# Performance work log

Measured on AMD Instinct MI355X. Metric: run time of the kernel, lower is better.

The kernel has to match this reference:

```python
import jax, jax.numpy as jnp
import numpy as np

N_ITER = 50  # bisection iterations (matches entmax_bisect default)


def entmax_bisect(x, alpha):
    """alpha-entmax via bisection along axis=1. x: [B, L, 1], alpha: [1] (>1)."""
    a_m1 = alpha - 1.0
    inv = 1.0 / a_m1
    xs = x * a_m1
    d = x.shape[1]
    max_val = jnp.max(xs, axis=1, keepdims=True)
    tau_lo = max_val - 1.0
    tau_hi = max_val - (1.0 / d) ** a_m1
    f_lo = jnp.sum(jnp.maximum(xs - tau_lo, 0.0) ** inv, axis=1, keepdims=True) - 1.0

    def body(i, carry):
        tau_lo, dm = carry
        dm = dm * 0.5
        tau_m = tau_lo + dm
        f_m = jnp.sum(jnp.maximum(xs - tau_m, 0.0) ** inv, axis=1, keepdims=True) - 1.0
        tau_lo = jnp.where(f_m * f_lo >= 0.0, tau_m, tau_lo)
        return (tau_lo, dm)

    tau_lo, dm = jax.lax.fori_loop(0, N_ITER, body, (tau_lo, tau_hi - tau_lo))
    p = jnp.maximum(xs - (tau_lo + 0.5 * dm), 0.0) ** inv
    return p / jnp.sum(p, axis=1, keepdims=True)


def setup_inputs() -> dict:
    key = jax.random.key(0)
    ks = jax.random.split(key, 8)
    B, L, E2, D = 256, 512, 512, 256  # E2 = emb_size * 2
    C_target = jax.random.normal(ks[0], (B, E2), jnp.float32)
    C = jax.random.normal(ks[1], (B, L, E2), jnp.float32)
    X = jax.random.normal(ks[2], (B, E2, D), jnp.float32)
    alpha = jnp.array([1.5], jnp.float32)  # entmax-1.5
    mask = jax.random.randint(ks[3], (B, L), 0, 2, jnp.int32).at[:, 0].set(1)
    s = 1.0 / np.sqrt(E2)
    Wg1 = jax.random.uniform(ks[4], (E2, E2), jnp.float32, -s, s)
    Wg2 = jax.random.uniform(ks[5], (E2, E2), jnp.float32, -s, s)
    Wg0 = jax.random.uniform(ks[6], (E2, 1), jnp.float32, -s, s)
    bias_alpha = jax.random.normal(ks[7], (E2,), jnp.float32) * 0.02
    return dict(C_target=C_target, C=C, X=X, alpha=alpha, mask=mask,
                Wg1=Wg1, Wg2=Wg2, Wg0=Wg0, bias_alpha=bias_alpha)


def reference(C_target, C, X, alpha, mask, Wg1, Wg2, Wg0, bias_alpha):
    q = C_target[:, None, :]                               # [B, 1, 2E]
    h = jax.nn.relu(C @ Wg1 + q @ Wg2 + bias_alpha)        # [B, L, 2E]
    score = h @ Wg0                                        # [B, L, 1]
    score = jnp.where(mask[..., None] == 0, -1e30, score)  # mask -> -inf
    p = entmax_bisect(score, alpha)                        # sparse attn over L
    attn = jnp.swapaxes(p, 1, 2) @ C                       # [B, 1, 2E]
    out = jnp.sum(attn @ X, axis=1)                        # [B, D]
    return out
```

## Files before the change

kernel.cpp:

```cpp
#include <hip/hip_runtime.h>
#include <hip/hip_bf16.h>

typedef __bf16 bf16_t;
typedef bf16_t bf16x8 __attribute__((ext_vector_type(8)));
typedef float f32x4 __attribute__((ext_vector_type(4)));

__global__ void k_wg1t(const float* __restrict__ Wg1, bf16_t* __restrict__ Wg1T) {
    __shared__ float tile[32][33];
    const int k0 = blockIdx.x * 32;
    const int e0 = blockIdx.y * 32;
    const int tx = threadIdx.x;
    const int ty = threadIdx.y;
    #pragma unroll
    for (int i = 0; i < 32; i += 8)
        tile[ty + i][tx] = Wg1[(k0 + ty + i) * 512 + e0 + tx];
    __syncthreads();
    #pragma unroll
    for (int i = 0; i < 32; i += 8)
        Wg1T[(e0 + ty + i) * 512 + k0 + tx] = (bf16_t)tile[tx][ty + i];
}

__global__ __launch_bounds__(256) void k_gate(const float* __restrict__ Ct,
                                              const float* __restrict__ Wg2,
                                              const float* __restrict__ bias,
                                              float* __restrict__ g) {
    __shared__ float q[512];
    const int b = blockIdx.x;
    const int t = threadIdx.x;
    q[t]       = Ct[b * 512 + t];
    q[t + 256] = Ct[b * 512 + t + 256];
    __syncthreads();
    const int e = (blockIdx.y << 8) + t;
    float acc = bias[e];
    #pragma unroll 8
    for (int k = 0; k < 512; ++k)
        acc = fmaf(q[k], Wg2[k * 512 + e], acc);
    g[b * 512 + e] = acc;
}

__global__ __launch_bounds__(256, 2) void k_score(const float* __restrict__ C,
                                                  const bf16_t* __restrict__ Wg1T,
                                                  const float* __restrict__ g,
                                                  const float* __restrict__ Wg0,
                                                  const int* __restrict__ mask,
                                                  float* __restrict__ score) {
    __shared__ bf16_t As[64 * 32];
    __shared__ bf16_t Bs[512 * 32];
    __shared__ float  sred[4][64];

    const int t    = threadIdx.x;
    const int lane = t & 63;
    const int wave = t >> 6;
    const int quad = lane >> 4;
    const int l15  = lane & 15;
    const int row0 = blockIdx.x * 64;
    const int b    = row0 >> 9;

    f32x4 acc[4][8] = {};

    for (int kc = 0; kc < 512; kc += 32) {
        __syncthreads();
        #pragma unroll
        for (int i = 0; i < 8; ++i) {
            const int f  = i * 256 + t;
            const int r  = f >> 2;
            const int c8 = (f & 3) << 3;
            __builtin_amdgcn_global_load_lds(
                (const __attribute__((address_space(1))) void*)(Wg1T + r * 512 + kc + c8),
                (__attribute__((address_space(3))) void*)(Bs + f * 8), 16, 0, 0);
        }
        #pragma unroll
        for (int i = 0; i < 2; ++i) {
            const int f  = i * 256 + t;
            const int r  = f >> 3;
            const int c4 = (f & 7) << 2;
            const float4 v = *reinterpret_cast<const float4*>(
                &C[(size_t)(row0 + r) * 512 + kc + c4]);
            union { bf16_t h[4]; uint2 u; } pk;
            pk.h[0] = (bf16_t)v.x; pk.h[1] = (bf16_t)v.y;
            pk.h[2] = (bf16_t)v.z; pk.h[3] = (bf16_t)v.w;
            *reinterpret_cast<uint2*>(&As[r * 32 + c4]) = pk.u;
        }
        __syncthreads();
        bf16x8 afr[4], bfr[8];
        #pragma unroll
        for (int mi = 0; mi < 4; ++mi)
            afr[mi] = *reinterpret_cast<const bf16x8*>(
                &As[(mi * 16 + l15) * 32 + quad * 8]);
        #pragma unroll
        for (int ni = 0; ni < 8; ++ni)
            bfr[ni] = *reinterpret_cast<const bf16x8*>(
                &Bs[(wave * 128 + ni * 16 + l15) * 32 + quad * 8]);
        #pragma unroll
        for (int mi = 0; mi < 4; ++mi)
            #pragma unroll
            for (int ni = 0; ni < 8; ++ni)
                acc[mi][ni] = __builtin_amdgcn_mfma_f32_16x16x32_bf16(
                    afr[mi], bfr[ni], acc[mi][ni], 0, 0, 0);
    }

    float rsum[16];
    #pragma unroll
    for (int i = 0; i < 16; ++i) rsum[i] = 0.f;
    #pragma unroll
    for (int ni = 0; ni < 8; ++ni) {
        const int n  = wave * 128 + ni * 16 + l15;
        const float gv = g[(b << 9) + n];
        const float w0 = Wg0[n];
        #pragma unroll
        for (int mi = 0; mi < 4; ++mi)
            #pragma unroll
            for (int r = 0; r < 4; ++r) {
                float u = fmaxf(acc[mi][ni][r] + gv, 0.f);
                rsum[mi * 4 + r] = fmaf(u, w0, rsum[mi * 4 + r]);
            }
    }
    #pragma unroll
    for (int i = 0; i < 16; ++i) {
        float v = rsum[i];
        v += __shfl_xor(v, 1);
        v += __shfl_xor(v, 2);
        v += __shfl_xor(v, 4);
        v += __shfl_xor(v, 8);
        rsum[i] = v;
    }
    if (l15 == 0) {
        #pragma unroll
        for (int mi = 0; mi < 4; ++mi)
            #pragma unroll
            for (int r = 0; r < 4; ++r)
                sred[wave][mi * 16 + quad * 4 + r] = rsum[mi * 4 + r];
    }
    __syncthreads();
    if (t < 64) {
        const float sc = sred[0][t] + sred[1][t] + sred[2][t] + sred[3][t];
        const int grow = row0 + t;
        score[grow] = (mask[grow] == 0) ? -1e30f : sc;
    }
}

__global__ __launch_bounds__(256) void k_entmax(const float* __restrict__ score,
                                                const float* __restrict__ alpha,
                                                float* __restrict__ p) {
    const int wave = threadIdx.x >> 6;
    const int lane = threadIdx.x & 63;
    const int b    = (blockIdx.x << 2) + wave;
    const float am1 = alpha[0] - 1.0f;
    const float inv = 1.0f / am1;
    const bool  sq  = fabsf(inv - 2.0f) < 1e-6f;

    const float* sb = score + (b << 9);
    float x[8];
    {
        const float4 v0 = *reinterpret_cast<const float4*>(sb + lane * 8);
        const float4 v1 = *reinterpret_cast<const float4*>(sb + lane * 8 + 4);
        x[0] = v0.x * am1; x[1] = v0.y * am1; x[2] = v0.z * am1; x[3] = v0.w * am1;
        x[4] = v1.x * am1; x[5] = v1.y * am1; x[6] = v1.z * am1; x[7] = v1.w * am1;
    }
    float m = x[0];
    #pragma unroll
    for (int j = 1; j < 8; ++j) m = fmaxf(m, x[j]);
    #pragma unroll
    for (int s = 1; s < 64; s <<= 1) m = fmaxf(m, __shfl_xor(m, s));

    float tau_lo = m - 1.0f;
    float dm = (m - powf(1.0f / 512.0f, am1)) - tau_lo;

    float f_lo;
    {
        float s = 0.f;
        #pragma unroll
        for (int j = 0; j < 8; ++j) {
            const float u = fmaxf(x[j] - tau_lo, 0.f);
            s += sq ? u * u : powf(u, inv);
        }
        #pragma unroll
        for (int sh = 1; sh < 64; sh <<= 1) s += __shfl_xor(s, sh);
        f_lo = s - 1.0f;
    }
    for (int it = 0; it < 50; ++it) {
        dm *= 0.5f;
        const float tau_m = tau_lo + dm;
        float s = 0.f;
        #pragma unroll
        for (int j = 0; j < 8; ++j) {
            const float u = fmaxf(x[j] - tau_m, 0.f);
            s += sq ? u * u : powf(u, inv);
        }
        #pragma unroll
        for (int sh = 1; sh < 64; sh <<= 1) s += __shfl_xor(s, sh);
        if ((s - 1.0f) * f_lo >= 0.f) tau_lo = tau_m;
    }
    const float tau = tau_lo + 0.5f * dm;
    float pj[8];
    float Z = 0.f;
    #pragma unroll
    for (int j = 0; j < 8; ++j) {
        const float u = fmaxf(x[j] - tau, 0.f);
        pj[j] = sq ? u * u : powf(u, inv);
        Z += pj[j];
    }
    #pragma unroll
    for (int sh = 1; sh < 64; sh <<= 1) Z += __shfl_xor(Z, sh);
    const float rz = 1.0f / Z;
    float4 o0, o1;
    o0.x = pj[0] * rz; o0.y = pj[1] * rz; o0.z = pj[2] * rz; o0.w = pj[3] * rz;
    o1.x = pj[4] * rz; o1.y = pj[5] * rz; o1.z = pj[6] * rz; o1.w = pj[7] * rz;
    *reinterpret_cast<float4*>(p + (b << 9) + lane * 8)     = o0;
    *reinterpret_cast<float4*>(p + (b << 9) + lane * 8 + 4) = o1;
}

__global__ __launch_bounds__(256) void k_attn(const float* __restrict__ p,
                                              const float* __restrict__ C,
                                              float* __restrict__ part) {
    __shared__ float pv_s[128];
    const int b  = blockIdx.x;
    const int ch = blockIdx.y;
    const int t  = threadIdx.x;
    const float* Cb = C + (size_t)b * 512 * 512 + (size_t)ch * 128 * 512;
    const float* pb = p + (b << 9) + (ch << 7);
    if (t < 128) pv_s[t] = pb[t];
    __syncthreads();
    float a0 = 0.f, a1 = 0.f;
    for (int l = 0; l < 128; ++l) {
        const float pv = pv_s[l];
        if (pv != 0.f) {
            a0 = fmaf(pv, Cb[(size_t)l * 512 + t], a0);
            a1 = fmaf(pv, Cb[(size_t)l * 512 + t + 256], a1);
        }
    }
    float* pp = part + (size_t)((b << 2) + ch) * 512;
    pp[t]       = a0;
    pp[t + 256] = a1;
}

__global__ __launch_bounds__(256) void k_out(const float* __restrict__ part,
                                             const float* __restrict__ X,
                                             float* __restrict__ out) {
    __shared__ float as_[128];
    const int b  = blockIdx.x;
    const int ec = blockIdx.y;
    const int t  = threadIdx.x;
    if (t < 128) {
        const int e = (ec << 7) + t;
        const float* pp = part + (size_t)(b << 2) * 512;
        as_[t] = pp[e] + pp[512 + e] + pp[1024 + e] + pp[1536 + e];
    }
    __syncthreads();
    const float* Xb = X + (size_t)b * 512 * 256 + (size_t)(ec << 7) * 256;
    float acc = 0.f;
    #pragma unroll 4
    for (int e = 0; e < 128; ++e)
        acc = fmaf(as_[e], Xb[e * 256 + t], acc);
    atomicAdd(&out[(b << 8) + t], acc);
}

extern "C" void kernel_launch(void* const* d_in, const int* in_sizes, int n_in,
                              void* d_out, int out_size, void* d_ws, size_t ws_size,
                              hipStream_t stream) {
    const float* C_target = (const float*)d_in[0];
    const float* C        = (const float*)d_in[1];
    const float* X        = (const float*)d_in[2];
    const float* alpha    = (const float*)d_in[3];
    const int*   mask     = (const int*)  d_in[4];
    const float* Wg1      = (const float*)d_in[5];
    const float* Wg2      = (const float*)d_in[6];
    const float* Wg0      = (const float*)d_in[7];
    const float* bias     = (const float*)d_in[8];
    float* out = (float*)d_out;

    char* ws = (char*)d_ws;
    bf16_t* wg1t  = (bf16_t*)(ws);
    float*  g     = (float*)(ws + (512u << 10));
    float*  score = (float*)(ws + (1024u << 10));
    float*  p     = (float*)(ws + (1536u << 10));
    float*  part  = (float*)(ws + (2048u << 10));

    k_wg1t  <<<dim3(16, 16), dim3(32, 8), 0, stream>>>(Wg1, wg1t);
    k_gate  <<<dim3(256, 2), 256, 0, stream>>>(C_target, Wg2, bias, g);
    k_score <<<2048, 256, 0, stream>>>(C, wg1t, g, Wg0, mask, score);
    k_entmax<<<64, 256, 0, stream>>>(score, alpha, p);
    k_attn  <<<dim3(256, 4), 256, 0, stream>>>(p, C, part);
    hipMemsetAsync(d_out, 0, (size_t)out_size * sizeof(float), stream);
    k_out   <<<dim3(256, 4), 256, 0, stream>>>(part, X, out);
}
```

Baseline: 593.8 us.

## Skip masked rows in score GEMM and use sparse entmax output for attention

Compacts the unmasked row indices per batch and computes the score GEMM only over those rows, gathering C rows by index. The N dimension is split across two blocks that combine through atomicAdd into a zeroed score buffer. Entmax now applies the mask itself and emits a compacted list of nonzero probabilities, so the attention pass gathers only rows with nonzero weight. This removes about half of the GEMM work, since the mask is random, and most of the C reads in attention. The costs are extra kernels, a memset, atomics and gathered, less regular memory access.

```diff
diff --git a/kernel.cpp b/kernel.cpp
--- a/kernel.cpp
+++ b/kernel.cpp
@@ -38,63 +38,106 @@
     g[b * 512 + e] = acc;
 }
 
-__global__ __launch_bounds__(256, 2) void k_score(const float* __restrict__ C,
+__global__ __launch_bounds__(64) void k_compact(const int* __restrict__ mask,
+                                                int* __restrict__ idx,
+                                                int* __restrict__ nnz) {
+    const int b    = blockIdx.x;
+    const int lane = threadIdx.x;
+    int base = 0;
+    #pragma unroll
+    for (int c = 0; c < 8; ++c) {
+        const int l = (c << 6) + lane;
+        const int v = mask[(b << 9) + l];
+        const unsigned long long m = __ballot(v != 0);
+        const int rank = __popcll(m & ((1ull << lane) - 1ull));
+        if (v) idx[(b << 9) + base + rank] = l;
+        base += __popcll(m);
+    }
+    if (lane == 0) nnz[b] = base;
+}
+
+__global__ __launch_bounds__(256, 3) void k_score(const float* __restrict__ C,
                                                   const bf16_t* __restrict__ Wg1T,
                                                   const float* __restrict__ g,
                                                   const float* __restrict__ Wg0,
-                                                  const int* __restrict__ mask,
+                                                  const int* __restrict__ idx,
+                                                  const int* __restrict__ nnz,
                                                   float* __restrict__ score) {
     __shared__ bf16_t As[64 * 32];
-    __shared__ bf16_t Bs[512 * 32];
+    __shared__ bf16_t Bs[256 * 32];
     __shared__ float  sred[4][64];
+    __shared__ int    rs[64];
 
     const int t    = threadIdx.x;
     const int lane = t & 63;
     const int wave = t >> 6;
     const int quad = lane >> 4;
     const int l15  = lane & 15;
-    const int row0 = blockIdx.x * 64;
-    const int b    = row0 >> 9;
-
-    f32x4 acc[4][8] = {};
+
+    const int bid  = blockIdx.x;
+    const int nh   = bid & 1;
+    const int tl   = bid >> 1;
+    const int b    = tl >> 3;
+    const int tile = tl & 7;
+    const int nb   = nnz[b];
+    if (tile * 64 >= nb) return;
+
+    if (t < 64) {
+        const int j = tile * 64 + t;
+        rs[t] = idx[(b << 9) + (j < nb ? j : nb - 1)];
+    }
+    __syncthreads();
+
+    const int r0 = t >> 3,        c0 = (t & 7) << 2;
+    const int r1 = 32 + (t >> 3);
+    const float* Cb  = C + ((size_t)b << 18);
+    const float* pa0 = Cb + (size_t)rs[r0] * 512 + c0;
+    const float* pa1 = Cb + (size_t)rs[r1] * 512 + c0;
+
+    float4 va0 = *reinterpret_cast<const float4*>(pa0);
+    float4 va1 = *reinterpret_cast<const float4*>(pa1);
+
+    const int ncol0 = nh << 8;
+    f32x4 acc[4][4] = {};
 
     for (int kc = 0; kc < 512; kc += 32) {
         __syncthreads();
         #pragma unroll
-        for (int i = 0; i < 8; ++i) {
+        for (int i = 0; i < 4; ++i) {
             const int f  = i * 256 + t;
             const int r  = f >> 2;
             const int c8 = (f & 3) << 3;
             __builtin_amdgcn_global_load_lds(
-                (const __attribute__((address_space(1))) void*)(Wg1T + r * 512 + kc + c8),
+                (const __attribute__((address_space(1))) void*)(Wg1T + (size_t)(ncol0 + r) * 512 + kc + c8),
                 (__attribute__((address_space(3))) void*)(Bs + f * 8), 16, 0, 0);
         }
-        #pragma unroll
-        for (int i = 0; i < 2; ++i) {
-            const int f  = i * 256 + t;
-            const int r  = f >> 3;
-            const int c4 = (f & 7) << 2;
-            const float4 v = *reinterpret_cast<const float4*>(
-                &C[(size_t)(row0 + r) * 512 + kc + c4]);
+        {
             union { bf16_t h[4]; uint2 u; } pk;
-            pk.h[0] = (bf16_t)v.x; pk.h[1] = (bf16_t)v.y;
-            pk.h[2] = (bf16_t)v.z; pk.h[3] = (bf16_t)v.w;
-            *reinterpret_cast<uint2*>(&As[r * 32 + c4]) = pk.u;
+            pk.h[0] = (bf16_t)va0.x; pk.h[1] = (bf16_t)va0.y;
+            pk.h[2] = (bf16_t)va0.z; pk.h[3] = (bf16_t)va0.w;
+            *reinterpret_cast<uint2*>(&As[r0 * 32 + c0]) = pk.u;
+            pk.h[0] = (bf16_t)va1.x; pk.h[1] = (bf16_t)va1.y;
+            pk.h[2] = (bf16_t)va1.z; pk.h[3] = (bf16_t)va1.w;
+            *reinterpret_cast<uint2*>(&As[r1 * 32 + c0]) = pk.u;
+        }
+        if (kc + 32 < 512) {
+            va0 = *reinterpret_cast<const float4*>(pa0 + kc + 32);
+            va1 = *reinterpret_cast<const float4*>(pa1 + kc + 32);
         }
         __syncthreads();
-        bf16x8 afr[4], bfr[8];
+        bf16x8 afr[4], bfr[4];
         #pragma unroll
         for (int mi = 0; mi < 4; ++mi)
             afr[mi] = *reinterpret_cast<const bf16x8*>(
                 &As[(mi * 16 + l15) * 32 + quad * 8]);
         #pragma unroll
-        for (int ni = 0; ni < 8; ++ni)
+        for (int ni = 0; ni < 4; ++ni)
             bfr[ni] = *reinterpret_cast<const bf16x8*>(
-                &Bs[(wave * 128 + ni * 16 + l15) * 32 + quad * 8]);
+                &Bs[(wave * 64 + ni * 16 + l15) * 32 + quad * 8]);
         #pragma unroll
         for (int mi = 0; mi < 4; ++mi)
             #pragma unroll
-            for (int ni = 0; ni < 8; ++ni)
+            for (int ni = 0; ni < 4; ++ni)
                 acc[mi][ni] = __builtin_amdgcn_mfma_f32_16x16x32_bf16(
                     afr[mi], bfr[ni], acc[mi][ni], 0, 0, 0);
     }
@@ -103,15 +146,15 @@
     #pragma unroll
     for (int i = 0; i < 16; ++i) rsum[i] = 0.f;
     #pragma unroll
-    for (int ni = 0; ni < 8; ++ni) {
-        const int n  = wave * 128 + ni * 16 + l15;
+    for (int ni = 0; ni < 4; ++ni) {
+        const int n  = ncol0 + wave * 64 + ni * 16 + l15;
         const float gv = g[(b << 9) + n];
         const float w0 = Wg0[n];
         #pragma unroll
         for (int mi = 0; mi < 4; ++mi)
             #pragma unroll
             for (int r = 0; r < 4; ++r) {
-                float u = fmaxf(acc[mi][ni][r] + gv, 0.f);
+                const float u = fmaxf(acc[mi][ni][r] + gv, 0.f);
                 rsum[mi * 4 + r] = fmaf(u, w0, rsum[mi * 4 + r]);
             }
     }
@@ -134,28 +177,36 @@
     __syncthreads();
     if (t < 64) {
         const float sc = sred[0][t] + sred[1][t] + sred[2][t] + sred[3][t];
-        const int grow = row0 + t;
-        score[grow] = (mask[grow] == 0) ? -1e30f : sc;
-    }
-}
-
-__global__ __launch_bounds__(256) void k_entmax(const float* __restrict__ score,
-                                                const float* __restrict__ alpha,
-                                                float* __restrict__ p) {
-    const int wave = threadIdx.x >> 6;
-    const int lane = threadIdx.x & 63;
-    const int b    = (blockIdx.x << 2) + wave;
+        if (tile * 64 + t < nb)
+            atomicAdd(&score[(b << 9) + rs[t]], sc);
+    }
+}
+
+__global__ __launch_bounds__(64) void k_entmax(const float* __restrict__ score,
+                                               const int* __restrict__ mask,
+                                               const float* __restrict__ alpha,
+                                               int* __restrict__ sidx,
+                                               float* __restrict__ sval,
+                                               int* __restrict__ snnz) {
+    const int lane = threadIdx.x;
+    const int b    = blockIdx.x;
     const float am1 = alpha[0] - 1.0f;
     const float inv = 1.0f / am1;
     const bool  sq  = fabsf(inv - 2.0f) < 1e-6f;
+    const float neg = -1e30f * am1;
 
     const float* sb = score + (b << 9);
+    const int*   mb = mask  + (b << 9);
     float x[8];
     {
         const float4 v0 = *reinterpret_cast<const float4*>(sb + lane * 8);
         const float4 v1 = *reinterpret_cast<const float4*>(sb + lane * 8 + 4);
-        x[0] = v0.x * am1; x[1] = v0.y * am1; x[2] = v0.z * am1; x[3] = v0.w * am1;
-        x[4] = v1.x * am1; x[5] = v1.y * am1; x[6] = v1.z * am1; x[7] = v1.w * am1;
+        const int4   m0 = *reinterpret_cast<const int4*>(mb + lane * 8);
+        const int4   m1 = *reinterpret_cast<const int4*>(mb + lane * 8 + 4);
+        x[0] = m0.x ? v0.x * am1 : neg; x[1] = m0.y ? v0.y * am1 : neg;
+        x[2] = m0.z ? v0.z * am1 : neg; x[3] = m0.w ? v0.w * am1 : neg;
+        x[4] = m1.x ? v1.x * am1 : neg; x[5] = m1.y ? v1.y * am1 : neg;
+        x[6] = m1.z ? v1.z * am1 : neg; x[7] = m1.w ? v1.w * am1 : neg;
     }
     float m = x[0];
     #pragma unroll
@@ -203,53 +254,63 @@
     #pragma unroll
     for (int sh = 1; sh < 64; sh <<= 1) Z += __shfl_xor(Z, sh);
     const float rz = 1.0f / Z;
-    float4 o0, o1;
-    o0.x = pj[0] * rz; o0.y = pj[1] * rz; o0.z = pj[2] * rz; o0.w = pj[3] * rz;
-    o1.x = pj[4] * rz; o1.y = pj[5] * rz; o1.z = pj[6] * rz; o1.w = pj[7] * rz;
-    *reinterpret_cast<float4*>(p + (b << 9) + lane * 8)     = o0;
-    *reinterpret_cast<float4*>(p + (b << 9) + lane * 8 + 4) = o1;
-}
-
-__global__ __launch_bounds__(256) void k_attn(const float* __restrict__ p,
+
+    int base = 0;
+    #pragma unroll
+    for (int j = 0; j < 8; ++j) {
+        const float pv = pj[j] * rz;
+        const unsigned long long bm = __ballot(pv > 0.f);
+        const int rank = __popcll(bm & ((1ull << lane) - 1ull));
+        if (pv > 0.f) {
+            sidx[(b << 9) + base + rank] = lane * 8 + j;
+            sval[(b << 9) + base + rank] = pv;
+        }
+        base += __popcll(bm);
+    }
+    if (lane == 0) snnz[b] = base;
+}
+
+__global__ __launch_bounds__(256) void k_attn(const int* __restrict__ sidx,
+                                              const float* __restrict__ sval,
+                                              const int* __restrict__ snnz,
                                               const float* __restrict__ C,
-                                              float* __restrict__ part) {
-    __shared__ float pv_s[128];
-    const int b  = blockIdx.x;
-    const int ch = blockIdx.y;
-    const int t  = threadIdx.x;
-    const float* Cb = C + (size_t)b * 512 * 512 + (size_t)ch * 128 * 512;
-    const float* pb = p + (b << 9) + (ch << 7);
-    if (t < 128) pv_s[t] = pb[t];
-    __syncthreads();
-    float a0 = 0.f, a1 = 0.f;
-    for (int l = 0; l < 128; ++l) {
-        const float pv = pv_s[l];
-        if (pv != 0.f) {
-            a0 = fmaf(pv, Cb[(size_t)l * 512 + t], a0);
-            a1 = fmaf(pv, Cb[(size_t)l * 512 + t + 256], a1);
-        }
-    }
-    float* pp = part + (size_t)((b << 2) + ch) * 512;
-    pp[t]       = a0;
-    pp[t + 256] = a1;
-}
-
-__global__ __launch_bounds__(256) void k_out(const float* __restrict__ part,
+                                              float* __restrict__ attn) {
+    __shared__ int   li[512];
+    __shared__ float lv[512];
+    const int b = blockIdx.x;
+    const int t = threadIdx.x;
+    const int e = (blockIdx.y << 8) + t;
+    const int n = snnz[b];
+    for (int i = t; i < n; i += 256) {
+        li[i] = sidx[(b << 9) + i];
+        lv[i] = sval[(b << 9) + i];
+    }
+    __syncthreads();
+    const float* Cb = C + ((size_t)b << 18);
+    float a = 0.f;
+    int j = 0;
+    for (; j + 8 <= n; j += 8) {
+        #pragma unroll
+        for (int u = 0; u < 8; ++u)
+            a = fmaf(lv[j + u], Cb[((size_t)li[j + u] << 9) + e], a);
+    }
+    for (; j < n; ++j)
+        a = fmaf(lv[j], Cb[((size_t)li[j] << 9) + e], a);
+    attn[(b << 9) + e] = a;
+}
+
+__global__ __launch_bounds__(256) void k_out(const float* __restrict__ attn,
                                              const float* __restrict__ X,
                                              float* __restrict__ out) {
     __shared__ float as_[128];
     const int b  = blockIdx.x;
     const int ec = blockIdx.y;
     const int t  = threadIdx.x;
-    if (t < 128) {
-        const int e = (ec << 7) + t;
-        const float* pp = part + (size_t)(b << 2) * 512;
-        as_[t] = pp[e] + pp[512 + e] + pp[1024 + e] + pp[1536 + e];
-    }
+    if (t < 128) as_[t] = attn[(b << 9) + (ec << 7) + t];
     __syncthreads();
     const float* Xb = X + (size_t)b * 512 * 256 + (size_t)(ec << 7) * 256;
     float acc = 0.f;
-    #pragma unroll 4
+    #pragma unroll 8
     for (int e = 0; e < 128; ++e)
         acc = fmaf(as_[e], Xb[e * 256 + t], acc);
     atomicAdd(&out[(b << 8) + t], acc);
@@ -271,16 +332,22 @@
 
     char* ws = (char*)d_ws;
     bf16_t* wg1t  = (bf16_t*)(ws);
-    float*  g     = (float*)(ws + (512u << 10));
+    float*  g     = (float*)(ws + ( 512u << 10));
     float*  score = (float*)(ws + (1024u << 10));
-    float*  p     = (float*)(ws + (1536u << 10));
-    float*  part  = (float*)(ws + (2048u << 10));
-
-    k_wg1t  <<<dim3(16, 16), dim3(32, 8), 0, stream>>>(Wg1, wg1t);
-    k_gate  <<<dim3(256, 2), 256, 0, stream>>>(C_target, Wg2, bias, g);
-    k_score <<<2048, 256, 0, stream>>>(C, wg1t, g, Wg0, mask, score);
-    k_entmax<<<64, 256, 0, stream>>>(score, alpha, p);
-    k_attn  <<<dim3(256, 4), 256, 0, stream>>>(p, C, part);
+    int*    idx   = (int*)  (ws + (1536u << 10));
+    int*    sidx  = (int*)  (ws + (2048u << 10));
+    float*  sval  = (float*)(ws + (2560u << 10));
+    float*  attn  = (float*)(ws + (3072u << 10));
+    int*    nnz   = (int*)  (ws + (3584u << 10));
+    int*    snnz  = (int*)  (ws + (3584u << 10) + 4096);
+
+    k_wg1t   <<<dim3(16, 16), dim3(32, 8), 0, stream>>>(Wg1, wg1t);
+    k_gate   <<<dim3(256, 2), 256, 0, stream>>>(C_target, Wg2, bias, g);
+    k_compact<<<256, 64, 0, stream>>>(mask, idx, nnz);
+    hipMemsetAsync(score, 0, 512u << 10, stream);
+    k_score  <<<4096, 256, 0, stream>>>(C, wg1t, g, Wg0, idx, nnz, score);
+    k_entmax <<<256, 64, 0, stream>>>(score, mask, alpha, sidx, sval, snnz);
+    k_attn   <<<dim3(256, 2), 256, 0, stream>>>(sidx, sval, snnz, C, attn);
     hipMemsetAsync(d_out, 0, (size_t)out_size * sizeof(float), stream);
-    k_out   <<<dim3(256, 4), 256, 0, stream>>>(part, X, out);
-}
+    k_out    <<<dim3(256, 4), 256, 0, stream>>>(attn, X, out);
+}
```

Result: slower. 611.6 us (+3.0%).
